# Optimization experiments

Measured on AMD Instinct MI355X. Metric: run time of the kernel, lower is better.

## Reference

```python
import jax, jax.numpy as jnp
import numpy as np
import math

# Static problem sizes (match input_specs)
B, TQ, SQ, TK, SK = 1, 8, 256, 32, 1024
DM, NH = 1024, 8
HD = DM // NH            # 128; mrope_section sums to HD//2
MROPE = [16, 24, 24]
ROPE_BASE = 10000.0


def _build_indices():
    """Reproduce create_idx_cube + slow/fast index selection (all static)."""
    T_max = max(TQ, TK)
    H_max = int(math.sqrt(max(SQ, SK)))
    cube = np.stack(np.meshgrid(np.arange(T_max), np.arange(H_max), np.arange(H_max), indexing='ij'), axis=-1)  # (T,H,W,3)
    # slow (query) indices
    t_idx = np.linspace(0, T_max - 1, TQ).astype(int)
    slow = cube[t_idx]
    if SQ < SK:
        h_q = int(math.sqrt(SQ))
        hi = np.linspace(0, H_max, 2 * h_q + 1).astype(int)[1:-1][::2]
        slow = slow[:, hi][:, :, hi]
    # fast (key) indices
    h_k = int(math.sqrt(SK))
    hf = np.linspace(0, H_max, 2 * h_k + 1).astype(int)[1:-1][::2]
    fast = cube[:, hf][:, :, hf]
    return slow.reshape(-1, 3).T, fast.reshape(-1, 3).T, max(T_max, H_max)


_slow_np, _fast_np, _SEQ = _build_indices()
SLOW_POS = jnp.asarray(_slow_np)   # (3, TQ*SQ) int
FAST_POS = jnp.asarray(_fast_np)   # (3, TK*SK) int

# Standard rotary tables: cos/sin of shape (seq_len, HD)
_inv = 1.0 / (ROPE_BASE ** (np.arange(0, HD, 2, dtype=np.float32) / HD))
_freqs = np.outer(np.arange(_SEQ, dtype=np.float32), _inv)
_emb = np.concatenate([_freqs, _freqs], axis=-1)
COS = jnp.asarray(np.cos(_emb), dtype=jnp.float32)
SIN = jnp.asarray(np.sin(_emb), dtype=jnp.float32)

# per-channel axis (t/h/w) selector, equivalent to the split/concat with i%3
AXIS_MAP = jnp.asarray(np.concatenate([np.full(m, i % 3) for i, m in enumerate(MROPE * 2)]))  # (HD,)


def rotate_half(x):
    return jnp.concatenate([-x[..., HD // 2:], x[..., :HD // 2]], axis=-1)


def apply_mrope(x, pos):
    # x: (B, NH, N, HD); pos: (3, N)
    cos_g = jnp.take_along_axis(COS[pos], AXIS_MAP[None, None, :], axis=0)[0]  # (N, HD)
    sin_g = jnp.take_along_axis(SIN[pos], AXIS_MAP[None, None, :], axis=0)[0]
    return x * cos_g[None, None] + rotate_half(x) * sin_g[None, None]


def setup_inputs() -> dict:
    key = jax.random.key(0)
    ks = jax.random.split(key, 9)
    s = 0.02
    return {
        'q': jax.random.normal(ks[0], (B, TQ, SQ, DM), jnp.float32),
        'k': jax.random.normal(ks[1], (B, TK, SK, DM), jnp.float32),
        'v': jax.random.normal(ks[2], (B, TK, SK, DM), jnp.float32),
        'Wq': jax.random.normal(ks[3], (DM, DM), jnp.float32) * s,
        'bq': jnp.zeros((DM,), jnp.float32),
        'Wk': jax.random.normal(ks[4], (DM, DM), jnp.float32) * s,
        'bk': jnp.zeros((DM,), jnp.float32),
        'Wv': jax.random.normal(ks[5], (DM, DM), jnp.float32) * s,
        'bv': jnp.zeros((DM,), jnp.float32),
    }


def reference(q, k, v, Wq, bq, Wk, bk, Wv, bv):
    # QKV projections -> (B, NH, N, HD)
    qh = (q.reshape(B, TQ * SQ, DM) @ Wq + bq).reshape(B, TQ * SQ, NH, HD).transpose(0, 2, 1, 3)
    kh = (k.reshape(B, TK * SK, DM) @ Wk + bk).reshape(B, TK * SK, NH, HD).transpose(0, 2, 1, 3)
    vh = (v.reshape(B, TK * SK, DM) @ Wv + bv).reshape(B, TK * SK, NH, HD).transpose(0, 2, 1, 3)
    # multimodal 3D RoPE on q (slow frames) and k (fast frames)
    qh = apply_mrope(qh, SLOW_POS)
    kh = apply_mrope(kh, FAST_POS)
    # group time: each query frame attends to its r = TK//TQ aligned kv frames
    r = TK // TQ
    qg = qh.reshape(NH, TQ, SQ, HD).transpose(1, 0, 2, 3)          # (TQ, NH, SQ, HD)
    kg = kh.reshape(NH, TQ, r * SK, HD).transpose(1, 0, 2, 3)      # (TQ, NH, r*SK, HD)
    vg = vh.reshape(NH, TQ, r * SK, HD).transpose(1, 0, 2, 3)
    scores = jnp.einsum('thqd,thkd->thqk', qg, kg) / math.sqrt(HD)
    attn = jax.nn.softmax(scores, axis=-1)
    out = jnp.einsum('thqk,thkd->thqd', attn, vg)                  # (TQ, NH, SQ, HD)
    return out.transpose(0, 2, 1, 3).reshape(B, TQ, SQ, DM)
```

## Files before the change

kernel.cpp:

```cpp
#include <hip/hip_runtime.h>

typedef __bf16 bf16;
typedef __bf16 bf16x8 __attribute__((ext_vector_type(8)));
typedef float  f32x4  __attribute__((ext_vector_type(4)));

#define MFMA16(a, b, c) __builtin_amdgcn_mfma_f32_16x16x32_bf16((a), (b), (c), 0, 0, 0)

#define GLOAD_LDS16(gptr, lptr)                                              \
    __builtin_amdgcn_global_load_lds(                                        \
        (const __attribute__((address_space(1))) unsigned int*)(gptr),       \
        (__attribute__((address_space(3))) unsigned int*)(lptr), 16, 0, 0)

constexpr int kDM = 1024;
constexpr int kNTOK = 32768;

static __device__ inline f32x4 zero4() { f32x4 z = {0.f, 0.f, 0.f, 0.f}; return z; }

__global__ __launch_bounds__(256) void cvt_bf16(
    const float* __restrict__ src, bf16* __restrict__ dst, int n8)
{
    int idx = blockIdx.x * 256 + threadIdx.x;
    const int stride = gridDim.x * 256;
    for (; idx < n8; idx += stride) {
        const float4 u0 = *(const float4*)(src + (size_t)idx * 8);
        const float4 u1 = *(const float4*)(src + (size_t)idx * 8 + 4);
        bf16x8 w;
        w[0] = (bf16)u0.x; w[1] = (bf16)u0.y; w[2] = (bf16)u0.z; w[3] = (bf16)u0.w;
        w[4] = (bf16)u1.x; w[5] = (bf16)u1.y; w[6] = (bf16)u1.z; w[7] = (bf16)u1.w;
        *(bf16x8*)&dst[(size_t)idx * 8] = w;
    }
}

__global__ __launch_bounds__(256) void transpose_all(
    const float* __restrict__ Wq, const float* __restrict__ Wk,
    const float* __restrict__ Wv, bf16* __restrict__ Wqt,
    bf16* __restrict__ Wkt, bf16* __restrict__ Wvt)
{
    __shared__ bf16 T[64][68];
    const float* W = (blockIdx.z == 0) ? Wq : (blockIdx.z == 1) ? Wk : Wv;
    bf16* Wt       = (blockIdx.z == 0) ? Wqt : (blockIdx.z == 1) ? Wkt : Wvt;
    const int tid = threadIdx.x;
    const int n0 = blockIdx.x * 64, k0 = blockIdx.y * 64;
    #pragma unroll
    for (int i = 0; i < 4; i++) {
        const int kk = (tid >> 4) + i * 16, nn4 = (tid & 15) * 4;
        float4 v = *(const float4*)&W[(size_t)(k0 + kk) * kDM + n0 + nn4];
        T[nn4 + 0][kk] = (bf16)v.x; T[nn4 + 1][kk] = (bf16)v.y;
        T[nn4 + 2][kk] = (bf16)v.z; T[nn4 + 3][kk] = (bf16)v.w;
    }
    __syncthreads();
    #pragma unroll
    for (int i = 0; i < 4; i++) {
        const int nn = (tid >> 4) + i * 16, kc = (tid & 15) * 4;
        *(ushort4*)&Wt[(size_t)(n0 + nn) * kDM + k0 + kc] = *(const ushort4*)&T[nn][kc];
    }
}

template <int MODE>
__global__ __launch_bounds__(256) void gemm_fused(
    const bf16* __restrict__ Xb, const bf16* __restrict__ Wt,
    const float* __restrict__ bias, bf16* __restrict__ out, int mtiles_per_xcd)
{
    __shared__ char smem[34816];
    bf16* Ab = (bf16*)smem;
    bf16* Bb = (bf16*)(smem + 16384);
    bf16* Y  = (bf16*)smem;

    const int b    = blockIdx.x;
    const int xcd  = b & 7;
    const int s    = b >> 3;
    const int m0   = (xcd * mtiles_per_xcd + (s >> 3)) * 128;
    const int n0   = (s & 7) * 128;
    const int tid  = threadIdx.x;
    const int wave = tid >> 6;
    const int lane = tid & 63;
    const int quad = lane >> 4, l16 = lane & 15;
    const int mb   = (wave & 1) * 64, nb = (wave >> 1) * 64;
    const int r8   = lane >> 3, j8 = lane & 7;

    f32x4 acc[4][4];
    #pragma unroll
    for (int i = 0; i < 4; i++)
        #pragma unroll
        for (int j = 0; j < 4; j++) acc[i][j] = zero4();

    for (int k0 = 0; k0 < kDM; k0 += 64) {
        __syncthreads();
        #pragma unroll
        for (int i = 0; i < 4; i++) {
            const int c = wave * 4 + i;
            const int row = c * 8 + r8;
            GLOAD_LDS16(&Xb[(size_t)(m0 + row) * kDM + k0 + ((j8 ^ (row & 7)) * 8)],
                        &Ab[c * 512]);
        }
        #pragma unroll
        for (int i = 0; i < 4; i++) {
            const int c = wave * 4 + i;
            const int row = c * 8 + r8;
            GLOAD_LDS16(&Wt[(size_t)(n0 + row) * kDM + k0 + ((j8 ^ (row & 7)) * 8)],
                        &Bb[c * 512]);
        }
        __syncthreads();
        #pragma unroll
        for (int ks = 0; ks < 2; ks++) {
            const int G = ks * 4 + quad;
            bf16x8 a[4], bfr[4];
            #pragma unroll
            for (int i = 0; i < 4; i++)
                a[i] = *(const bf16x8*)&Ab[(mb + i * 16 + l16) * 64 + ((G ^ (l16 & 7)) * 8)];
            #pragma unroll
            for (int j = 0; j < 4; j++)
                bfr[j] = *(const bf16x8*)&Bb[(nb + j * 16 + l16) * 64 + ((G ^ (l16 & 7)) * 8)];
            #pragma unroll
            for (int i = 0; i < 4; i++)
                #pragma unroll
                for (int j = 0; j < 4; j++)
                    acc[i][j] = MFMA16(a[i], bfr[j], acc[i][j]);
        }
    }

    __syncthreads();

    if (MODE == 3) {
        #pragma unroll
        for (int j = 0; j < 4; j++) {
            const int n = nb + j * 16 + l16;
            const float bv = bias[n0 + n];
            #pragma unroll
            for (int i = 0; i < 4; i++) {
                const int m = mb + i * 16 + quad * 4;
                bf16 tmp[4];
                #pragma unroll
                for (int r = 0; r < 4; r++) tmp[r] = (bf16)(acc[i][j][r] + bv);
                *(ushort4*)&Y[n * 136 + m] = *(const ushort4*)tmp;
            }
        }
        __syncthreads();
        const int row = tid >> 1, seg = (tid & 1) * 64;
        #pragma unroll
        for (int kk = 0; kk < 8; kk++)
            *(uint4*)&out[(size_t)(n0 + row) * kNTOK + m0 + seg + kk * 8] =
                *(const uint4*)&Y[row * 136 + seg + kk * 8];
    } else {
        if (wave >= 2) {
            #pragma unroll
            for (int j = 0; j < 4; j++) {
                const int dcol = 64 + j * 16 + l16;
                const float bv = bias[n0 + dcol];
                #pragma unroll
                for (int i = 0; i < 4; i++)
                    #pragma unroll
                    for (int r = 0; r < 4; r++)
                        Y[(mb + i * 16 + quad * 4 + r) * 136 + dcol] =
                            (bf16)(acc[i][j][r] + bv);
            }
        }
        __syncthreads();
        if (wave < 2) {
            #pragma unroll
            for (int j = 0; j < 4; j++) {
                const int d = j * 16 + l16;
                const float bv = bias[n0 + d];
                const float invf = exp2f((float)d * -0.20762050593045951f);
                #pragma unroll
                for (int i = 0; i < 4; i++) {
                    #pragma unroll
                    for (int r = 0; r < 4; r++) {
                        const int mloc = mb + i * 16 + quad * 4 + r;
                        const int tok = m0 + mloc;
                        int pt, ph, pw;
                        if (MODE == 2) { pt = tok >> 10; ph = (tok >> 5) & 31; pw = tok & 31; }
                        else { int tq = tok >> 8; pt = (31 * tq) / 7;
                               ph = 2 * ((tok >> 4) & 15) + 1; pw = 2 * (tok & 15) + 1; }
                        const int p = (d < 16) ? pt : ((d < 40) ? ph : pw);
                        float sn, cs;
                        __sincosf((float)p * invf, &sn, &cs);
                        const float x1 = acc[i][j][r] + bv;
                        const float x2 = (float)Y[mloc * 136 + 64 + d];
                        Y[mloc * 136 + d]      = (bf16)(x1 * cs - x2 * sn);
                        Y[mloc * 136 + 64 + d] = (bf16)(x2 * cs + x1 * sn);
                    }
                }
            }
        }
        __syncthreads();
        const int row = tid >> 1, seg = (tid & 1) * 64;
        #pragma unroll
        for (int kk = 0; kk < 8; kk++)
            *(uint4*)&out[(size_t)(m0 + row) * kDM + n0 + seg + kk * 8] =
                *(const uint4*)&Y[row * 136 + seg + kk * 8];
    }
}

__global__ __launch_bounds__(256) void attn_kernel(
    const bf16* __restrict__ qh, const bf16* __restrict__ kh,
    const bf16* __restrict__ vt, float* __restrict__ Opart, float* __restrict__ ml)
{
    __shared__ bf16 Ks[64 * 128];
    __shared__ bf16 Vs[128 * 64];
    __shared__ bf16 Ps[4][16][64];

    const int tid  = threadIdx.x;
    const int z    = blockIdx.x, h = blockIdx.y, qb = blockIdx.z;
    const int t    = z >> 2, sp = z & 3;
    const int wave = tid >> 6;
    const int lane = tid & 63;
    const int quad = lane >> 4, l16 = lane & 15;

    const int qrow = qb * 64 + wave * 16 + l16;
    const size_t qbase = ((size_t)(t * 256 + qrow)) * kDM + h * 128;
    bf16x8 aq[4];
    #pragma unroll
    for (int kb = 0; kb < 4; kb++)
        aq[kb] = *(const bf16x8*)&qh[qbase + kb * 32 + quad * 8];

    bf16x8 ones;
    #pragma unroll
    for (int e = 0; e < 8; e++) ones[e] = (bf16)1.0f;

    f32x4 o[9];
    #pragma unroll
    for (int j = 0; j < 9; j++) o[j] = zero4();
    float m_run[4];
    #pragma unroll
    for (int r = 0; r < 4; r++) m_run[r] = -1e30f;
    const float scale = 0.08838834764831845f;

    const int r16 = lane >> 4, j16 = lane & 15;
    const int r8  = lane >> 3, j8  = lane & 7;

    for (int kt = 0; kt < 16; kt++) {
        const int kbase = t * 4096 + sp * 1024 + kt * 64;
        __syncthreads();
        #pragma unroll
        for (int i = 0; i < 4; i++) {
            const int c = wave * 4 + i;
            const int krow = c * 4 + r16;
            GLOAD_LDS16(&kh[(size_t)(kbase + krow) * kDM + h * 128 + ((j16 ^ (krow & 15)) * 8)],
                        &Ks[c * 512]);
        }
        #pragma unroll
        for (int i = 0; i < 4; i++) {
            const int c = wave * 4 + i;
            GLOAD_LDS16(&vt[(size_t)(h * 128 + c * 8 + r8) * kNTOK + kbase + ((j8 ^ r8) * 8)],
                        &Vs[c * 512]);
        }
        __syncthreads();

        f32x4 s[4];
        #pragma unroll
        for (int c = 0; c < 4; c++) s[c] = zero4();
        __builtin_amdgcn_s_setprio(1);
        #pragma unroll
        for (int kb = 0; kb < 4; kb++) {
            #pragma unroll
            for (int c = 0; c < 4; c++) {
                bf16x8 b = *(const bf16x8*)&Ks[(c * 16 + l16) * 128 + (((kb * 4 + quad) ^ l16) * 8)];
                s[c] = MFMA16(aq[kb], b, s[c]);
            }
        }
        __builtin_amdgcn_s_setprio(0);

        float alpha[4];
        #pragma unroll
        for (int r = 0; r < 4; r++) {
            float sv[4];
            #pragma unroll
            for (int c = 0; c < 4; c++) sv[c] = s[c][r] * scale;
            float mx = fmaxf(fmaxf(sv[0], sv[1]), fmaxf(sv[2], sv[3]));
            #pragma unroll
            for (int off = 1; off < 16; off <<= 1) mx = fmaxf(mx, __shfl_xor(mx, off));
            const float mn = fmaxf(m_run[r], mx);
            alpha[r] = __expf(m_run[r] - mn);
            m_run[r] = mn;
            const int q7 = quad * 4 + r;
            #pragma unroll
            for (int c = 0; c < 4; c++) {
                const int col = (c * 16 + l16) ^ ((q7 & 7) * 8);
                Ps[wave][q7][col] = (bf16)__expf(sv[c] - mn);
            }
        }
        #pragma unroll
        for (int j = 0; j < 9; j++)
            #pragma unroll
            for (int r = 0; r < 4; r++) o[j][r] *= alpha[r];
        __builtin_amdgcn_s_setprio(1);
        #pragma unroll
        for (int ks = 0; ks < 2; ks++) {
            bf16x8 pa = *(const bf16x8*)&Ps[wave][l16][((ks * 4 + quad) ^ (l16 & 7)) * 8];
            #pragma unroll
            for (int j = 0; j < 8; j++) {
                bf16x8 bv = *(const bf16x8*)&Vs[(j * 16 + l16) * 64 + (((ks * 4 + quad) ^ (l16 & 7)) * 8)];
                o[j] = MFMA16(pa, bv, o[j]);
            }
            o[8] = MFMA16(pa, ones, o[8]);
        }
        __builtin_amdgcn_s_setprio(0);
    }

    #pragma unroll
    for (int r = 0; r < 4; r++) {
        const int srow = qb * 64 + wave * 16 + quad * 4 + r;
        const size_t pr = ((size_t)(z * 8 + h)) * 256 + srow;
        #pragma unroll
        for (int j = 0; j < 8; j++)
            Opart[pr * 128 + j * 16 + l16] = o[j][r];
        if (l16 == 0) { ml[pr * 2] = m_run[r]; ml[pr * 2 + 1] = o[8][r]; }
    }
}

__global__ __launch_bounds__(256) void combine_kernel(
    const float* __restrict__ Opart, const float* __restrict__ ml,
    float* __restrict__ out)
{
    const int tid = threadIdx.x;
    const int rid = blockIdx.x * 2 + (tid >> 7);
    const int d   = tid & 127;
    const int t = rid >> 11, h = (rid >> 8) & 7, srow = rid & 255;

    float mv[4], lv[4];
    #pragma unroll
    for (int sp = 0; sp < 4; sp++) {
        const size_t pr = ((size_t)((t * 4 + sp) * 8 + h)) * 256 + srow;
        float2 p = *(const float2*)&ml[pr * 2];
        mv[sp] = p.x; lv[sp] = p.y;
    }
    const float ms = fmaxf(fmaxf(mv[0], mv[1]), fmaxf(mv[2], mv[3]));
    float lsum = 0.f, acc = 0.f;
    #pragma unroll
    for (int sp = 0; sp < 4; sp++) {
        const size_t pr = ((size_t)((t * 4 + sp) * 8 + h)) * 256 + srow;
        const float w = __expf(mv[sp] - ms);
        lsum += lv[sp] * w;
        acc  += Opart[pr * 128 + d] * w;
    }
    out[((size_t)(t * 256 + srow)) * kDM + h * 128 + d] = acc / lsum;
}

extern "C" void kernel_launch(void* const* d_in, const int* in_sizes, int n_in,
                              void* d_out, int out_size, void* d_ws, size_t ws_size,
                              hipStream_t stream)
{
    const float* q  = (const float*)d_in[0];
    const float* k  = (const float*)d_in[1];
    const float* v  = (const float*)d_in[2];
    const float* Wq = (const float*)d_in[3];
    const float* bq = (const float*)d_in[4];
    const float* Wk = (const float*)d_in[5];
    const float* bk = (const float*)d_in[6];
    const float* Wv = (const float*)d_in[7];
    const float* bv = (const float*)d_in[8];
    float* out = (float*)d_out;

    bf16* qh  = (bf16*)d_ws;
    bf16* kh  = qh + (size_t)2048 * 1024;
    bf16* vt  = kh + (size_t)32768 * 1024;
    bf16* Wqt = vt + (size_t)32768 * 1024;
    bf16* Wkt = Wqt + (size_t)1024 * 1024;
    bf16* Wvt = Wkt + (size_t)1024 * 1024;
    float* Opart = (float*)(Wvt + (size_t)1024 * 1024);
    float* ml    = Opart + (size_t)32 * 8 * 256 * 128;
    bf16* Xb     = (bf16*)(ml + (size_t)32 * 8 * 256 * 2);

    transpose_all<<<dim3(16, 16, 3), 256, 0, stream>>>(Wq, Wk, Wv, Wqt, Wkt, Wvt);

    cvt_bf16<<<512, 256, 0, stream>>>(q, Xb, 2048 * 1024 / 8);
    gemm_fused<1><<<128,  256, 0, stream>>>(Xb, Wqt, bq, qh, 2);

    cvt_bf16<<<2048, 256, 0, stream>>>(k, Xb, 32768 * 1024 / 8);
    gemm_fused<2><<<2048, 256, 0, stream>>>(Xb, Wkt, bk, kh, 32);

    cvt_bf16<<<2048, 256, 0, stream>>>(v, Xb, 32768 * 1024 / 8);
    gemm_fused<3><<<2048, 256, 0, stream>>>(Xb, Wvt, bv, vt, 32);

    attn_kernel<<<dim3(32, 8, 4), 256, 0, stream>>>(qh, kh, vt, Opart, ml);
    combine_kernel<<<8192, 256, 0, stream>>>(Opart, ml, out);
}
```

Before: 635.3 us.

## Double-buffer LDS tiles in projection GEMM to overlap loads with MFMA

The QKV projection GEMM now uses two 32KB LDS buffers and prefetches the next K-slice via global_load_lds while computing MFMAs on the current one. A single wait and barrier per iteration replaces the two syncthreads. This is meant to hide global memory latency behind compute. The cost is doubled LDS use (64KB), which may reduce occupancy.

```diff
diff --git a/kernel.cpp b/kernel.cpp
--- a/kernel.cpp
+++ b/kernel.cpp
@@ -61,10 +61,8 @@
     const bf16* __restrict__ Xb, const bf16* __restrict__ Wt,
     const float* __restrict__ bias, bf16* __restrict__ out, int mtiles_per_xcd)
 {
-    __shared__ char smem[34816];
-    bf16* Ab = (bf16*)smem;
-    bf16* Bb = (bf16*)(smem + 16384);
-    bf16* Y  = (bf16*)smem;
+    __shared__ char smem[65536];
+    bf16* Y = (bf16*)smem;
 
     const int b    = blockIdx.x;
     const int xcd  = b & 7;
@@ -84,23 +82,30 @@
         #pragma unroll
         for (int j = 0; j < 4; j++) acc[i][j] = zero4();
 
-    for (int k0 = 0; k0 < kDM; k0 += 64) {
-        __syncthreads();
+    auto stage = [&](int k0, char* buf) {
+        bf16* Ab = (bf16*)buf;
+        bf16* Bb = (bf16*)(buf + 16384);
         #pragma unroll
         for (int i = 0; i < 4; i++) {
             const int c = wave * 4 + i;
             const int row = c * 8 + r8;
-            GLOAD_LDS16(&Xb[(size_t)(m0 + row) * kDM + k0 + ((j8 ^ (row & 7)) * 8)],
-                        &Ab[c * 512]);
-        }
-        #pragma unroll
-        for (int i = 0; i < 4; i++) {
-            const int c = wave * 4 + i;
-            const int row = c * 8 + r8;
-            GLOAD_LDS16(&Wt[(size_t)(n0 + row) * kDM + k0 + ((j8 ^ (row & 7)) * 8)],
-                        &Bb[c * 512]);
-        }
-        __syncthreads();
+            const int off = (j8 ^ (row & 7)) * 8;
+            GLOAD_LDS16(&Xb[(size_t)(m0 + row) * kDM + k0 + off], &Ab[c * 512]);
+            GLOAD_LDS16(&Wt[(size_t)(n0 + row) * kDM + k0 + off], &Bb[c * 512]);
+        }
+    };
+
+    stage(0, smem);
+    asm volatile("s_waitcnt vmcnt(0)" ::: "memory");
+    __builtin_amdgcn_s_barrier();
+
+    for (int t = 0; t < 16; ++t) {
+        const char* cur = smem + (t & 1) * 32768;
+        if (t < 15) stage((t + 1) * 64, smem + ((t + 1) & 1) * 32768);
+        __builtin_amdgcn_sched_barrier(0);
+
+        const bf16* Ab = (const bf16*)cur;
+        const bf16* Bb = (const bf16*)(cur + 16384);
         #pragma unroll
         for (int ks = 0; ks < 2; ks++) {
             const int G = ks * 4 + quad;
@@ -117,6 +122,10 @@
                 for (int j = 0; j < 4; j++)
                     acc[i][j] = MFMA16(a[i], bfr[j], acc[i][j]);
         }
+
+        if (t < 15) asm volatile("s_waitcnt vmcnt(0)" ::: "memory");
+        __builtin_amdgcn_sched_barrier(0);
+        __builtin_amdgcn_s_barrier();
     }
 
     __syncthreads();
```

New measurement: 621.6 us. 2.2% less time.
